# Kernel optimization log

Hardware: AMD Instinct MI355X
Metric: run time of the kernel (lower is better)

The kernel has to match this reference:

```python
import jax, jax.numpy as jnp
import numpy as np

N_CLASS, N_SUPPORT, N_QUERY = 64, 5, 64
D_IN, C, WIN = 1024, 128, 5
D = C * WIN * WIN  # 3200, fine-encoder output dim


def setup_inputs() -> dict:
    key = jax.random.key(0)
    ks = jax.random.split(key, 6)
    s = 0.02  # weight init scale
    return {
        "xs": jax.random.normal(ks[0], (N_CLASS, N_SUPPORT, D_IN), jnp.float32),
        "xq": jax.random.normal(ks[1], (N_CLASS, N_QUERY, D_IN), jnp.float32),
        "W_share": jax.random.normal(ks[2], (D_IN, D), jnp.float32) * s,
        "b_share": jnp.zeros((D,), jnp.float32),
        "W_att": jax.random.normal(ks[3], (C, C), jnp.float32) * s,
        "b_att": jnp.zeros((C,), jnp.float32),
        "W_fine": jax.random.normal(ks[4], (D, D), jnp.float32) * s,
        "b_fine": jnp.zeros((D,), jnp.float32),
    }


def reference(xs, xq, W_share, b_share, W_att, b_att, W_fine, b_fine):
    n_class, n_support = xs.shape[0], xs.shape[1]
    n_query = xq.shape[1]
    ns = n_class * n_support

    # concat support + query, run shared encoder
    x = jnp.concatenate([xs.reshape(ns, -1), xq.reshape(n_class * n_query, -1)], axis=0)
    z_share = jax.nn.relu(x @ W_share + b_share)            # [N, D]
    z4 = z_share.reshape(-1, C, WIN, WIN)

    # attention head: spatial mean -> linear -> per-channel logits
    z_att = z4.mean(axis=(2, 3)) @ W_att + b_att            # [N, C]

    diag_c = jax.nn.softmax(z_att[:ns].mean(axis=0)) * C    # [C]
    w = jnp.repeat(diag_c, WIN * WIN)                       # [D] diagonal of learned metric

    # fine encoder (flatten + linear)
    z = z_share @ W_fine + b_fine                           # [N, D]
    z_proto = z[:ns].reshape(n_class, n_support, -1).mean(axis=1)  # [n_class, D]
    zq = z[ns:]                                             # [n, D]

    # attentionMetric with diagonal metric == weighted squared distance:
    # dists[i,j] = sum_d w_d (zq_i - proto_j)^2, expanded to avoid the n*m*d diff tensor
    q2 = (zq * zq) @ w                                      # [n]
    p2 = (z_proto * z_proto) @ w                            # [m]
    cross = (zq * w) @ z_proto.T                            # [n, m]
    dists = q2[:, None] + p2[None, :] - 2.0 * cross         # [n, m]

    log_p_y = jax.nn.log_softmax(-dists, axis=1).reshape(n_class, n_query, n_class)
    target = jnp.arange(n_class)
    tgt = jnp.broadcast_to(target[:, None, None], (n_class, n_query, 1))
    loss_val = -jnp.take_along_axis(log_p_y, tgt, axis=2).mean()
    y_hat = jnp.argmax(log_p_y, axis=2)
    acc_val = (y_hat == target[:, None]).astype(jnp.float32).mean()
    return loss_val, acc_val
```

## Files before the change

kernel.cpp:

```cpp
#include <hip/hip_runtime.h>
#include <math.h>

#define N_CLASS 64
#define N_SUPPORT 5
#define N_QUERY 64
#define D_IN 1024
#define C_CH 128
#define WIN 5
#define D_FEAT 3200
#define NS 320
#define NQ 4096
#define M_ROWS 4416
#define M_PAD8 4608
#define N_PAD8 3328

#define ZP_SLICE  (N_CLASS * D_FEAT)
#define GT_SLICE  (128 * D_FEAT)
#define CR_SLICE  (NQ * 128)
#define NKS       10
#define LOSS_BLKS (NQ / 4)

#define PREP_X   4608
#define PREP_WS  3200
#define PREP_WZ  128
#define CONV_WF  10000

#define WS_SCALE    64.0f
#define WS_INVSCALE 0.015625f

#define WS_XF8      0u
#define WS_WSF8     4718592u
#define WS_ZSB      8126464u
#define WS_WFB      36388864u
#define WS_WFTB     56868864u
#define WS_ARENA    77348864u
#define WS_UB       98320384u
#define WS_YB       99139584u
#define WS_GT       99958784u
#define WS_WV       100777984u
#define WS_P2       100790784u
#define WS_CVEC     100791296u
#define WS_LPART    100791808u

typedef __bf16 bf16x8 __attribute__((ext_vector_type(8)));
typedef __bf16 bf16x4 __attribute__((ext_vector_type(4)));
typedef float floatx4 __attribute__((ext_vector_type(4)));
typedef __attribute__((address_space(1))) const void* gptr_t;
typedef __attribute__((address_space(3))) void* lptr_t;

__device__ __forceinline__ float waveReduceSum(float v) {
    for (int off = 32; off > 0; off >>= 1) v += __shfl_xor(v, off, 64);
    return v;
}

__global__ __launch_bounds__(256) void prep_kernel(const float* __restrict__ xs,
                                                   const float* __restrict__ xq,
                                                   const float* __restrict__ W_share,
                                                   unsigned char* __restrict__ Xf8,
                                                   unsigned char* __restrict__ Wsf8)
{
    __shared__ float tile[32][33];
    const int b = blockIdx.x;
    const int t = threadIdx.x;

    if (b < PREP_X) {
        const int e = (b * 256 + t) * 4;
        const int row = e >> 10;
        const int col = e & 1023;
        float4 v = make_float4(0.f, 0.f, 0.f, 0.f);
        if (row < NS)          v = *(const float4*)(xs + (size_t)row * D_IN + col);
        else if (row < M_ROWS) v = *(const float4*)(xq + (size_t)(row - NS) * D_IN + col);
        int p = __builtin_amdgcn_cvt_pk_fp8_f32(v.x, v.y, 0, false);
        p     = __builtin_amdgcn_cvt_pk_fp8_f32(v.z, v.w, p, true);
        const int ocol = col ^ (((row >> 1) & 1) << 3);
        *(int*)(Xf8 + (size_t)row * D_IN + ocol) = p;
        return;
    }
    if (b < PREP_X + PREP_WS) {
        const int tx = t & 31;
        const int ty = t >> 5;
        const int tb = b - PREP_X;
        const int n0 = (tb % 100) * 32;
        const int k0 = (tb / 100) * 32;
#pragma unroll
        for (int i = ty; i < 32; i += 8)
            tile[i][tx] = W_share[(size_t)(k0 + i) * D_FEAT + n0 + tx];
        __syncthreads();
#pragma unroll
        for (int i = ty; i < 32; i += 8) {
            const int p = __builtin_amdgcn_cvt_pk_fp8_f32(tile[tx][i] * WS_SCALE, 0.f,
                                                          0, false);
            const int n = n0 + i;
            const int k = (k0 + tx) ^ (((n >> 1) & 1) << 3);
            Wsf8[(size_t)n * D_IN + k] = (unsigned char)(p & 0xff);
        }
        return;
    }
    const int r = b - (PREP_X + PREP_WS);
    ((int*)(Wsf8 + (size_t)(3200 + r) * D_IN))[t] = 0;
}

__global__ __launch_bounds__(512, 2) void gemm_fp8_8p(const unsigned char* __restrict__ A,
                                                      const unsigned char* __restrict__ Bt,
                                                      const float* __restrict__ bias,
                                                      __bf16* __restrict__ out_bf)
{
    __shared__ __align__(16) unsigned char smem[131072];

    const int t    = threadIdx.x;
    const int lane = t & 63;
    const int w    = t >> 6;
    const int wm   = w >> 2;
    const int wn   = w & 3;

    const int bx = blockIdx.x % 13;
    const int by = blockIdx.x / 13;
    const int bm = by * 256;
    const int bn = bx * 256;

    const int q    = lane >> 4;
    const int r16  = lane & 15;
    const int m3   = (r16 >> 1) & 7;
    const int off0 = (q ^ m3) * 8;

    const int rowA = (wm * 128 + r16) * 64;
    const int rowB = (wn * 64 + r16) * 64;

    const int srow  = t >> 2;
    const int sunit = 16 * ((t & 3) ^ ((srow >> 2) & 3));

    auto stage_a = [&](int uu) {
        const unsigned char* g = A + (size_t)(bm + srow) * D_IN + uu * 64 + sunit;
        unsigned char* l = smem + (uu & 3) * 32768 + t * 16;
        __builtin_amdgcn_global_load_lds((gptr_t)g,            (lptr_t)l,          16, 0, 0);
        __builtin_amdgcn_global_load_lds((gptr_t)(g + 131072), (lptr_t)(l + 8192), 16, 0, 0);
    };
    auto stage_b = [&](int uu) {
        const unsigned char* g = Bt + (size_t)(bn + srow) * D_IN + uu * 64 + sunit;
        unsigned char* l = smem + (uu & 3) * 32768 + 16384 + t * 16;
        __builtin_amdgcn_global_load_lds((gptr_t)g,            (lptr_t)l,          16, 0, 0);
        __builtin_amdgcn_global_load_lds((gptr_t)(g + 131072), (lptr_t)(l + 8192), 16, 0, 0);
    };

    floatx4 acc[8][4] = {};
    long av[8], bv[4];

    auto ld_frags = [&](const unsigned char* sa, int o) {
        const unsigned char* sb = sa + 16384;
#pragma unroll
        for (int mi = 0; mi < 8; ++mi) av[mi] = *(const long*)(sa + rowA + mi * 1024 + o);
#pragma unroll
        for (int ni = 0; ni < 4; ++ni) bv[ni] = *(const long*)(sb + rowB + ni * 1024 + o);
    };
    auto do_mfma = [&]() {
        __builtin_amdgcn_s_barrier();
        asm volatile("s_waitcnt lgkmcnt(0)" ::: "memory");
        __builtin_amdgcn_s_setprio(1);
#pragma unroll
        for (int mi = 0; mi < 8; ++mi)
#pragma unroll
            for (int ni = 0; ni < 4; ++ni)
                acc[mi][ni] = __builtin_amdgcn_mfma_f32_16x16x32_fp8_fp8(
                    av[mi], bv[ni], acc[mi][ni], 0, 0, 0);
        __builtin_amdgcn_s_setprio(0);
        __builtin_amdgcn_s_barrier();
    };

    stage_a(0); stage_b(0);
    stage_a(1); stage_b(1);
    stage_a(2); stage_b(2);

    for (int u = 0; u < 13; ++u) {
        const unsigned char* sa = smem + (u & 3) * 32768;
        asm volatile("s_waitcnt vmcnt(8)" ::: "memory");
        __builtin_amdgcn_s_barrier();
        ld_frags(sa, off0);
        stage_a(u + 3);
        do_mfma();
        ld_frags(sa, off0 ^ 32);
        stage_b(u + 3);
        do_mfma();
    }
    asm volatile("s_waitcnt vmcnt(0)" ::: "memory");
    __builtin_amdgcn_s_barrier();
    for (int u = 13; u < 16; ++u) {
        const unsigned char* sa = smem + (u & 3) * 32768;
        ld_frags(sa, off0);
        do_mfma();
        ld_frags(sa, off0 ^ 32);
        do_mfma();
    }

#pragma unroll
    for (int ni = 0; ni < 4; ++ni) {
        const int col = bn + wn * 64 + ni * 16 + r16;
        if (col < D_FEAT) {
            const float bcol = bias[col];
#pragma unroll
            for (int mi = 0; mi < 8; ++mi) {
#pragma unroll
                for (int reg = 0; reg < 4; ++reg) {
                    const int row = bm + wm * 128 + mi * 16 + q * 4 + reg;
                    if (row < M_ROWS) {
                        float v = acc[mi][ni][reg] * WS_INVSCALE + bcol;
                        v = fmaxf(v, 0.f);
                        out_bf[(size_t)row * D_FEAT + col] = (__bf16)v;
                    }
                }
            }
        }
    }
}

__global__ __launch_bounds__(256) void gemm_bf16(const __bf16* __restrict__ A,
                                                 const __bf16* __restrict__ Bt,
                                                 const float* __restrict__ bias,
                                                 __bf16* __restrict__ out_bf,
                                                 float* __restrict__ out_f32,
                                                 int N, int strideK, int kIters,
                                                 int Mout, int relu, int sliceStride,
                                                 int nbx, int nby)
{
    __shared__ __align__(16) char smem[32768];

    int bx, by, ks;
    {
        const int nbxy = nbx * nby;
        ks = blockIdx.x / nbxy;
        const int b = blockIdx.x - ks * nbxy;
        const int fg = nbx >> 3;
        const int full = fg * 8 * nby;
        if (b < full) {
            const int g = b / (8 * nby);
            const int r = b - g * 8 * nby;
            bx = g * 8 + (r & 7);
            by = r >> 3;
        } else {
            const int rem = nbx - fg * 8;
            const int r = b - full;
            bx = fg * 8 + r % rem;
            by = r / rem;
        }
    }

    const int t    = threadIdx.x;
    const int lane = t & 63;
    const int w    = t >> 6;
    const int wm   = w >> 1;
    const int wn   = w & 1;
    const int bm   = by * 128;
    const int bn   = bx * 128;

    const int q    = lane >> 4;
    const int r16  = lane & 15;
    const int sw   = (r16 >> 1) & 3;
    const int cA   = (q ^ sw) * 8;

    const int srow   = w * 16 + (lane >> 2);
    const int sglob8 = (((lane & 3) ^ ((lane >> 3) & 3))) * 8;

    const int kBase = ks * kIters * 64;
    floatx4 acc[4][4] = {};

    for (int ki = 0; ki < kIters; ++ki) {
        const int k0 = kBase + ki * 64;
        __syncthreads();
#pragma unroll
        for (int s = 0; s < 2; ++s) {
#pragma unroll
            for (int j = 0; j < 2; ++j) {
                const __bf16* ga = A  + (size_t)(bm + j * 64 + srow) * strideK
                                      + k0 + s * 32 + sglob8;
                const __bf16* gb = Bt + (size_t)(bn + j * 64 + srow) * strideK
                                      + k0 + s * 32 + sglob8;
                char* la = smem +         s * 8192 + (j * 256 + w * 64) * 16;
                char* lb = smem + 16384 + s * 8192 + (j * 256 + w * 64) * 16;
                __builtin_amdgcn_global_load_lds((gptr_t)ga, (lptr_t)la, 16, 0, 0);
                __builtin_amdgcn_global_load_lds((gptr_t)gb, (lptr_t)lb, 16, 0, 0);
            }
        }
        __syncthreads();

#pragma unroll
        for (int s = 0; s < 2; ++s) {
            const __bf16* sAe = (const __bf16*)(smem +         s * 8192);
            const __bf16* sBe = (const __bf16*)(smem + 16384 + s * 8192);
            bf16x8 av[4], bv[4];
#pragma unroll
            for (int mi = 0; mi < 4; ++mi)
                av[mi] = *(const bf16x8*)(sAe + ((wm * 64 + mi * 16 + r16) * 32 + cA));
#pragma unroll
            for (int ni = 0; ni < 4; ++ni)
                bv[ni] = *(const bf16x8*)(sBe + ((wn * 64 + ni * 16 + r16) * 32 + cA));
#pragma unroll
            for (int mi = 0; mi < 4; ++mi)
#pragma unroll
                for (int ni = 0; ni < 4; ++ni)
                    acc[mi][ni] = __builtin_amdgcn_mfma_f32_16x16x32_bf16(
                        av[mi], bv[ni], acc[mi][ni], 0, 0, 0);
        }
    }

#pragma unroll
    for (int ni = 0; ni < 4; ++ni) {
        const int col = bn + wn * 64 + ni * 16 + r16;
        const float bcol = sliceStride ? 0.f : bias[col];
#pragma unroll
        for (int mi = 0; mi < 4; ++mi) {
#pragma unroll
            for (int reg = 0; reg < 4; ++reg) {
                const int row = bm + wm * 64 + mi * 16 + q * 4 + reg;
                if (row < Mout) {
                    if (sliceStride) {
                        out_f32[(size_t)ks * sliceStride + (size_t)row * N + col] =
                            acc[mi][ni][reg];
                    } else {
                        float v = acc[mi][ni][reg] + bcol;
                        if (relu) v = fmaxf(v, 0.f);
                        if (out_f32) out_f32[(size_t)row * N + col] = v;
                        else         out_bf [(size_t)row * N + col] = (__bf16)v;
                    }
                }
            }
        }
    }
}

__global__ __launch_bounds__(256) void ut_conv_kernel(const __bf16* __restrict__ z_share,
                                                      const float* __restrict__ W_fine,
                                                      __bf16* __restrict__ u,
                                                      float* __restrict__ upool,
                                                      __bf16* __restrict__ Wfb,
                                                      __bf16* __restrict__ WfTb)
{
    __shared__ __align__(16) char smem_u[D_FEAT * 4];
    const int b = blockIdx.x;
    const int t = threadIdx.x;

    if (b >= 128) {
        float (*tile)[33] = (float(*)[33])smem_u;
        const int tb = b - 128;
        const int tx = t & 31;
        const int ty = t >> 5;
        const int n0 = (tb % 100) * 32;
        const int k0 = (tb / 100) * 32;
#pragma unroll
        for (int i = ty; i < 32; i += 8) {
            const float v = W_fine[(size_t)(k0 + i) * D_FEAT + n0 + tx];
            Wfb[(size_t)(k0 + i) * D_FEAT + n0 + tx] = (__bf16)v;
            tile[i][tx] = v;
        }
        __syncthreads();
#pragma unroll
        for (int i = ty; i < 32; i += 8)
            WfTb[(size_t)(n0 + i) * D_FEAT + k0 + tx] = (__bf16)tile[tx][i];
        return;
    }

    float* srow_ = (float*)smem_u;
    const int p = b;
    if (p >= N_CLASS) {
        for (int k = t; k < D_FEAT; k += 256) u[(size_t)p * D_FEAT + k] = (__bf16)0.f;
        return;
    }
    const __bf16* base = z_share + (size_t)(p * N_SUPPORT) * D_FEAT;
    for (int k = t; k < D_FEAT; k += 256) {
        float s = 0.f;
#pragma unroll
        for (int ss = 0; ss < N_SUPPORT; ++ss) s += (float)base[(size_t)ss * D_FEAT + k];
        s *= (1.0f / N_SUPPORT);
        u[(size_t)p * D_FEAT + k] = (__bf16)s;
        srow_[k] = s;
    }
    __syncthreads();
    if (t < C_CH) {
        float pool = 0.f;
#pragma unroll
        for (int win = 0; win < 25; ++win) pool += srow_[t * 25 + win];
        upool[(size_t)p * C_CH + t] = pool;
    }
}

__global__ __launch_bounds__(128) void att2_kernel(const float* __restrict__ upool,
                                                   const float* __restrict__ W_att,
                                                   const float* __restrict__ b_att,
                                                   float* __restrict__ wvec)
{
    __shared__ float s_pm[C_CH];
    __shared__ float s_att[C_CH];
    __shared__ float s_diag[C_CH];
    const int c = threadIdx.x;
    float a = 0.f;
    for (int p = 0; p < N_CLASS; ++p) a += upool[(size_t)p * C_CH + c];
    s_pm[c] = a * (1.0f / (N_CLASS * 25));
    __syncthreads();
    float acc = b_att[c];
    for (int k = 0; k < C_CH; ++k) acc += s_pm[k] * W_att[k * C_CH + c];
    s_att[c] = acc;
    __syncthreads();
    float m = -INFINITY;
    for (int k = 0; k < C_CH; ++k) m = fmaxf(m, s_att[k]);
    float s = 0.f;
    for (int k = 0; k < C_CH; ++k) s += expf(s_att[k] - m);
    s_diag[c] = expf(acc - m) / s * (float)C_CH;
    __syncthreads();
    for (int j = c; j < D_FEAT; j += C_CH) wvec[j] = s_diag[j / 25];
}

__global__ __launch_bounds__(256) void y_kernel(const float* __restrict__ zp_part,
                                                const float* __restrict__ wv,
                                                const float* __restrict__ bf,
                                                __bf16* __restrict__ y,
                                                float* __restrict__ p2,
                                                float* __restrict__ cvec)
{
    __shared__ float s_red2[8];
    const int p = blockIdx.x;
    const int t = threadIdx.x;
    if (p >= N_CLASS) {
        for (int j = t; j < D_FEAT; j += 256) y[(size_t)p * D_FEAT + j] = (__bf16)0.f;
        return;
    }
    float s2 = 0.f, sc = 0.f;
    for (int j = t; j < D_FEAT; j += 256) {
        float zpf = bf[j];
#pragma unroll
        for (int ss = 0; ss < NKS; ++ss)
            zpf += zp_part[(size_t)ss * ZP_SLICE + (size_t)p * D_FEAT + j];
        const float wj = wv[j];
        y[(size_t)p * D_FEAT + j] = (__bf16)(wj * zpf);
        s2 += wj * zpf * zpf;
        sc += bf[j] * wj * zpf;
    }
    s2 = waveReduceSum(s2);
    sc = waveReduceSum(sc);
    const int lane = t & 63, wid = t >> 6;
    if (lane == 0) { s_red2[wid] = s2; s_red2[4 + wid] = sc; }
    __syncthreads();
    if (t == 0) {
        p2[p]   = s_red2[0] + s_red2[1] + s_red2[2] + s_red2[3];
        cvec[p] = s_red2[4] + s_red2[5] + s_red2[6] + s_red2[7];
    }
}

__global__ __launch_bounds__(256) void gtsum_kernel(const float* __restrict__ gp,
                                                    __bf16* __restrict__ Gt)
{
    const int i4 = blockIdx.x * 256 + threadIdx.x;
    if (i4 >= GT_SLICE / 4) return;
    float4 s = make_float4(0.f, 0.f, 0.f, 0.f);
#pragma unroll
    for (int ss = 0; ss < NKS; ++ss) {
        const float4 v = *(const float4*)(gp + (size_t)ss * GT_SLICE + i4 * 4);
        s.x += v.x; s.y += v.y; s.z += v.z; s.w += v.w;
    }
    bf16x4 o = { (__bf16)s.x, (__bf16)s.y, (__bf16)s.z, (__bf16)s.w };
    *(bf16x4*)(Gt + (size_t)i4 * 4) = o;
}

__global__ __launch_bounds__(256) void loss_kernel(const float* __restrict__ cross_part,
                                                   const float* __restrict__ p2,
                                                   const float* __restrict__ cvec,
                                                   float* __restrict__ lpart)
{
    __shared__ float s_l[4], s_a[4];
    const int t = threadIdx.x;
    const int lane = t & 63, wid = t >> 6;
    const int i = blockIdx.x * 4 + wid;
    float cr = 0.f;
#pragma unroll
    for (int ss = 0; ss < NKS; ++ss)
        cr += cross_part[(size_t)ss * CR_SLICE + (size_t)i * 128 + lane];
    const float neg = 2.0f * (cr + cvec[lane]) - p2[lane];
    float m = neg;
    for (int off = 32; off > 0; off >>= 1) m = fmaxf(m, __shfl_xor(m, off, 64));
    float e = expf(neg - m);
    float ssum = e;
    for (int off = 32; off > 0; off >>= 1) ssum += __shfl_xor(ssum, off, 64);
    const float lse = m + logf(ssum);
    const int tcls = i >> 6;
    const float negt = __shfl(neg, tcls, 64);
    float v = -neg; int bi = lane;
    for (int off = 32; off > 0; off >>= 1) {
        const float ov = __shfl_xor(v, off, 64);
        const int   oi = __shfl_xor(bi, off, 64);
        if (ov < v || (ov == v && oi < bi)) { v = ov; bi = oi; }
    }
    if (lane == 0) { s_l[wid] = lse - negt; s_a[wid] = (bi == tcls) ? 1.0f : 0.0f; }
    __syncthreads();
    if (t == 0) {
        lpart[blockIdx.x]             = s_l[0] + s_l[1] + s_l[2] + s_l[3];
        lpart[LOSS_BLKS + blockIdx.x] = s_a[0] + s_a[1] + s_a[2] + s_a[3];
    }
}

__global__ __launch_bounds__(256) void writeout_kernel(const float* __restrict__ lpart,
                                                       float* __restrict__ out)
{
    __shared__ float s_red2[8];
    const int t = threadIdx.x;
    float l = 0.f, a = 0.f;
    for (int k = t; k < LOSS_BLKS; k += 256) {
        l += lpart[k];
        a += lpart[LOSS_BLKS + k];
    }
    l = waveReduceSum(l);
    a = waveReduceSum(a);
    const int lane = t & 63, wid = t >> 6;
    if (lane == 0) { s_red2[wid] = l; s_red2[4 + wid] = a; }
    __syncthreads();
    if (t == 0) {
        out[0] = (s_red2[0] + s_red2[1] + s_red2[2] + s_red2[3]) * (1.0f / NQ);
        out[1] = (s_red2[4] + s_red2[5] + s_red2[6] + s_red2[7]) * (1.0f / NQ);
    }
}

extern "C" void kernel_launch(void* const* d_in, const int* in_sizes, int n_in,
                              void* d_out, int out_size, void* d_ws, size_t ws_size,
                              hipStream_t stream)
{
    const float* xs      = (const float*)d_in[0];
    const float* xq      = (const float*)d_in[1];
    const float* W_share = (const float*)d_in[2];
    const float* b_share = (const float*)d_in[3];
    const float* W_att   = (const float*)d_in[4];
    const float* b_att   = (const float*)d_in[5];
    const float* W_fine  = (const float*)d_in[6];
    const float* b_fine  = (const float*)d_in[7];
    float* out = (float*)d_out;

    char* ws = (char*)d_ws;
    unsigned char* Xf8  = (unsigned char*)(ws + WS_XF8);
    unsigned char* Wsf8 = (unsigned char*)(ws + WS_WSF8);
    __bf16* Zsb     = (__bf16*)(ws + WS_ZSB);
    __bf16* Wfb     = (__bf16*)(ws + WS_WFB);
    __bf16* WfTb    = (__bf16*)(ws + WS_WFTB);
    float*  arena   = (float*) (ws + WS_ARENA);
    float*  upool   = arena;
    float*  zp_part = arena;
    float*  gt_part = arena;
    float*  cr_part = arena;
    __bf16* ub      = (__bf16*)(ws + WS_UB);
    __bf16* yb      = (__bf16*)(ws + WS_YB);
    __bf16* Gt      = (__bf16*)(ws + WS_GT);
    float*  wv      = (float*) (ws + WS_WV);
    float*  p2v     = (float*) (ws + WS_P2);
    float*  cvec    = (float*) (ws + WS_CVEC);
    float*  lpart   = (float*) (ws + WS_LPART);

    prep_kernel<<<PREP_X + PREP_WS + PREP_WZ, 256, 0, stream>>>(xs, xq, W_share,
                                                                Xf8, Wsf8);

    gemm_fp8_8p<<<18 * 13, 512, 0, stream>>>(Xf8, Wsf8, b_share, Zsb);

    ut_conv_kernel<<<128 + CONV_WF, 256, 0, stream>>>(Zsb, W_fine, ub, upool,
                                                      Wfb, WfTb);
    att2_kernel<<<1, C_CH, 0, stream>>>(upool, W_att, b_att, wv);

    gemm_bf16<<<25 * NKS, 256, 0, stream>>>(
        ub, WfTb, nullptr, nullptr, zp_part,
        D_FEAT, D_FEAT, 5, N_CLASS, 0, ZP_SLICE, 25, 1);

    y_kernel<<<128, 256, 0, stream>>>(zp_part, wv, b_fine, yb, p2v, cvec);

    gemm_bf16<<<25 * NKS, 256, 0, stream>>>(
        yb, Wfb, nullptr, nullptr, gt_part,
        D_FEAT, D_FEAT, 5, 128, 0, GT_SLICE, 25, 1);

    gtsum_kernel<<<(GT_SLICE / 4 + 255) / 256, 256, 0, stream>>>(gt_part, Gt);

    gemm_bf16<<<32 * NKS, 256, 0, stream>>>(
        Zsb + (size_t)NS * D_FEAT, Gt, nullptr, nullptr, cr_part,
        128, D_FEAT, 5, NQ, 0, CR_SLICE, 1, 32);

    loss_kernel<<<LOSS_BLKS, 256, 0, stream>>>(cr_part, p2v, cvec, lpart);

    writeout_kernel<<<1, 256, 0, stream>>>(lpart, out);
}
```

Baseline: 253.7 us.

## Retile FP8 shared-encoder GEMM to 128x128 blocks with LDS-staged coalesced epilogue

```diff
diff --git a/kernel.cpp b/kernel.cpp
--- a/kernel.cpp
+++ b/kernel.cpp
@@ -11,8 +11,7 @@
 #define NS 320
 #define NQ 4096
 #define M_ROWS 4416
-#define M_PAD8 4608
-#define N_PAD8 3328
+#define M_PAD 4480
 
 #define ZP_SLICE  (N_CLASS * D_FEAT)
 #define GT_SLICE  (128 * D_FEAT)
@@ -20,9 +19,8 @@
 #define NKS       10
 #define LOSS_BLKS (NQ / 4)
 
-#define PREP_X   4608
+#define PREP_X   4480
 #define PREP_WS  3200
-#define PREP_WZ  128
 #define CONV_WF  10000
 
 #define WS_SCALE    64.0f
@@ -76,138 +74,154 @@
         *(int*)(Xf8 + (size_t)row * D_IN + ocol) = p;
         return;
     }
-    if (b < PREP_X + PREP_WS) {
-        const int tx = t & 31;
-        const int ty = t >> 5;
-        const int tb = b - PREP_X;
-        const int n0 = (tb % 100) * 32;
-        const int k0 = (tb / 100) * 32;
-#pragma unroll
-        for (int i = ty; i < 32; i += 8)
-            tile[i][tx] = W_share[(size_t)(k0 + i) * D_FEAT + n0 + tx];
-        __syncthreads();
-#pragma unroll
-        for (int i = ty; i < 32; i += 8) {
-            const int p = __builtin_amdgcn_cvt_pk_fp8_f32(tile[tx][i] * WS_SCALE, 0.f,
-                                                          0, false);
-            const int n = n0 + i;
-            const int k = (k0 + tx) ^ (((n >> 1) & 1) << 3);
-            Wsf8[(size_t)n * D_IN + k] = (unsigned char)(p & 0xff);
-        }
-        return;
-    }
-    const int r = b - (PREP_X + PREP_WS);
-    ((int*)(Wsf8 + (size_t)(3200 + r) * D_IN))[t] = 0;
-}
-
-__global__ __launch_bounds__(512, 2) void gemm_fp8_8p(const unsigned char* __restrict__ A,
-                                                      const unsigned char* __restrict__ Bt,
-                                                      const float* __restrict__ bias,
-                                                      __bf16* __restrict__ out_bf)
-{
-    __shared__ __align__(16) unsigned char smem[131072];
+    const int tx = t & 31;
+    const int ty = t >> 5;
+    const int tb = b - PREP_X;
+    const int n0 = (tb % 100) * 32;
+    const int k0 = (tb / 100) * 32;
+#pragma unroll
+    for (int i = ty; i < 32; i += 8)
+        tile[i][tx] = W_share[(size_t)(k0 + i) * D_FEAT + n0 + tx];
+    __syncthreads();
+#pragma unroll
+    for (int i = ty; i < 32; i += 8) {
+        const int p = __builtin_amdgcn_cvt_pk_fp8_f32(tile[tx][i] * WS_SCALE, 0.f,
+                                                      0, false);
+        const int n = n0 + i;
+        const int k = (k0 + tx) ^ (((n >> 1) & 1) << 3);
+        Wsf8[(size_t)n * D_IN + k] = (unsigned char)(p & 0xff);
+    }
+}
+
+__global__ __launch_bounds__(256, 3) void gemm_fp8_128(const unsigned char* __restrict__ A,
+                                                       const unsigned char* __restrict__ Bt,
+                                                       const float* __restrict__ bias,
+                                                       __bf16* __restrict__ out_bf)
+{
+    __shared__ __align__(16) unsigned char smem[49152];
 
     const int t    = threadIdx.x;
     const int lane = t & 63;
     const int w    = t >> 6;
-    const int wm   = w >> 2;
-    const int wn   = w & 3;
-
-    const int bx = blockIdx.x % 13;
-    const int by = blockIdx.x / 13;
-    const int bm = by * 256;
-    const int bn = bx * 256;
+    const int wm   = w >> 1;
+    const int wn   = w & 1;
+
+    const int bx = blockIdx.x % 25;
+    const int by = blockIdx.x / 25;
+    const int bm = by * 128;
+    const int bn = bx * 128;
 
     const int q    = lane >> 4;
     const int r16  = lane & 15;
     const int m3   = (r16 >> 1) & 7;
     const int off0 = (q ^ m3) * 8;
 
-    const int rowA = (wm * 128 + r16) * 64;
+    const int rowA = (wm * 64 + r16) * 64;
     const int rowB = (wn * 64 + r16) * 64;
 
     const int srow  = t >> 2;
     const int sunit = 16 * ((t & 3) ^ ((srow >> 2) & 3));
 
-    auto stage_a = [&](int uu) {
-        const unsigned char* g = A + (size_t)(bm + srow) * D_IN + uu * 64 + sunit;
-        unsigned char* l = smem + (uu & 3) * 32768 + t * 16;
-        __builtin_amdgcn_global_load_lds((gptr_t)g,            (lptr_t)l,          16, 0, 0);
-        __builtin_amdgcn_global_load_lds((gptr_t)(g + 131072), (lptr_t)(l + 8192), 16, 0, 0);
+    const unsigned char* gA = A  + (size_t)(bm + srow) * D_IN + sunit;
+    const unsigned char* gB = Bt + (size_t)(bn + srow) * D_IN + sunit;
+
+    auto stage = [&](int uu, int slot) {
+        const unsigned char* ga = gA + uu * 64;
+        const unsigned char* gb = gB + uu * 64;
+        unsigned char* l = smem + slot * 16384 + t * 16;
+        __builtin_amdgcn_global_load_lds((gptr_t)ga,           (lptr_t)l,            16, 0, 0);
+        __builtin_amdgcn_global_load_lds((gptr_t)(ga + 65536), (lptr_t)(l + 4096),   16, 0, 0);
+        __builtin_amdgcn_global_load_lds((gptr_t)gb,           (lptr_t)(l + 8192),   16, 0, 0);
+        __builtin_amdgcn_global_load_lds((gptr_t)(gb + 65536), (lptr_t)(l + 12288),  16, 0, 0);
     };
-    auto stage_b = [&](int uu) {
-        const unsigned char* g = Bt + (size_t)(bn + srow) * D_IN + uu * 64 + sunit;
-        unsigned char* l = smem + (uu & 3) * 32768 + 16384 + t * 16;
-        __builtin_amdgcn_global_load_lds((gptr_t)g,            (lptr_t)l,          16, 0, 0);
-        __builtin_amdgcn_global_load_lds((gptr_t)(g + 131072), (lptr_t)(l + 8192), 16, 0, 0);
+
+    floatx4 acc[4][4] = {};
+    long av[4], bv[4];
+
+    auto ld_frags = [&](const unsigned char* sa, int o) {
+#pragma unroll
+        for (int mi = 0; mi < 4; ++mi)
+            av[mi] = *(const long*)(sa + rowA + mi * 1024 + o);
+#pragma unroll
+        for (int ni = 0; ni < 4; ++ni)
+            bv[ni] = *(const long*)(sa + 8192 + rowB + ni * 1024 + o);
     };
-
-    floatx4 acc[8][4] = {};
-    long av[8], bv[4];
-
-    auto ld_frags = [&](const unsigned char* sa, int o) {
-        const unsigned char* sb = sa + 16384;
-#pragma unroll
-        for (int mi = 0; mi < 8; ++mi) av[mi] = *(const long*)(sa + rowA + mi * 1024 + o);
-#pragma unroll
-        for (int ni = 0; ni < 4; ++ni) bv[ni] = *(const long*)(sb + rowB + ni * 1024 + o);
+    auto mfma16 = [&]() {
+#pragma unroll
+        for (int mi = 0; mi < 4; ++mi)
+#pragma unroll
+            for (int ni = 0; ni < 4; ++ni)
+                acc[mi][ni] = __builtin_amdgcn_mfma_f32_16x16x32_fp8_fp8(
+                    av[mi], bv[ni], acc[mi][ni], 0, 0, 0);
     };
-    auto do_mfma = [&]() {
+
+    stage(0, 0);
+    stage(1, 1);
+    asm volatile("s_waitcnt vmcnt(4)" ::: "memory");
+    __builtin_amdgcn_s_barrier();
+
+    int sl = 0;
+    for (int u = 0; u < 14; ++u) {
+        const unsigned char* sa = smem + sl * 16384;
+        ld_frags(sa, off0);
+        stage(u + 2, sl == 0 ? 2 : sl - 1);
         __builtin_amdgcn_s_barrier();
         asm volatile("s_waitcnt lgkmcnt(0)" ::: "memory");
         __builtin_amdgcn_s_setprio(1);
-#pragma unroll
-        for (int mi = 0; mi < 8; ++mi)
-#pragma unroll
-            for (int ni = 0; ni < 4; ++ni)
-                acc[mi][ni] = __builtin_amdgcn_mfma_f32_16x16x32_fp8_fp8(
-                    av[mi], bv[ni], acc[mi][ni], 0, 0, 0);
+        mfma16();
         __builtin_amdgcn_s_setprio(0);
         __builtin_amdgcn_s_barrier();
-    };
-
-    stage_a(0); stage_b(0);
-    stage_a(1); stage_b(1);
-    stage_a(2); stage_b(2);
-
-    for (int u = 0; u < 13; ++u) {
-        const unsigned char* sa = smem + (u & 3) * 32768;
-        asm volatile("s_waitcnt vmcnt(8)" ::: "memory");
+        ld_frags(sa, off0 ^ 32);
+        asm volatile("s_waitcnt vmcnt(4)" ::: "memory");
         __builtin_amdgcn_s_barrier();
-        ld_frags(sa, off0);
-        stage_a(u + 3);
-        do_mfma();
-        ld_frags(sa, off0 ^ 32);
-        stage_b(u + 3);
-        do_mfma();
+        asm volatile("s_waitcnt lgkmcnt(0)" ::: "memory");
+        __builtin_amdgcn_s_setprio(1);
+        mfma16();
+        __builtin_amdgcn_s_setprio(0);
+        __builtin_amdgcn_s_barrier();
+        sl = sl == 2 ? 0 : sl + 1;
+    }
+    {
+        const unsigned char* sa = smem + sl * 16384;
+        ld_frags(sa, off0);       mfma16();
+        ld_frags(sa, off0 ^ 32);  mfma16();
+        sl = sl == 2 ? 0 : sl + 1;
     }
     asm volatile("s_waitcnt vmcnt(0)" ::: "memory");
     __builtin_amdgcn_s_barrier();
-    for (int u = 13; u < 16; ++u) {
-        const unsigned char* sa = smem + (u & 3) * 32768;
-        ld_frags(sa, off0);
-        do_mfma();
-        ld_frags(sa, off0 ^ 32);
-        do_mfma();
-    }
-
-#pragma unroll
-    for (int ni = 0; ni < 4; ++ni) {
-        const int col = bn + wn * 64 + ni * 16 + r16;
-        if (col < D_FEAT) {
-            const float bcol = bias[col];
-#pragma unroll
-            for (int mi = 0; mi < 8; ++mi) {
-#pragma unroll
-                for (int reg = 0; reg < 4; ++reg) {
-                    const int row = bm + wm * 128 + mi * 16 + q * 4 + reg;
-                    if (row < M_ROWS) {
-                        float v = acc[mi][ni][reg] * WS_INVSCALE + bcol;
-                        v = fmaxf(v, 0.f);
-                        out_bf[(size_t)row * D_FEAT + col] = (__bf16)v;
-                    }
-                }
+    {
+        const unsigned char* sa = smem + sl * 16384;
+        ld_frags(sa, off0);       mfma16();
+        ld_frags(sa, off0 ^ 32);  mfma16();
+    }
+
+    __syncthreads();
+    float bcol[4];
+#pragma unroll
+    for (int ni = 0; ni < 4; ++ni) bcol[ni] = bias[bn + wn * 64 + ni * 16 + r16];
+    const int ebase = (wm * 64 + q * 4) * 256 + wn * 128 + r16 * 2;
+#pragma unroll
+    for (int mi = 0; mi < 4; ++mi)
+#pragma unroll
+        for (int ni = 0; ni < 4; ++ni) {
+            const int cb = (ni ^ q) << 5;
+#pragma unroll
+            for (int reg = 0; reg < 4; ++reg) {
+                float v = acc[mi][ni][reg] * WS_INVSCALE + bcol[ni];
+                v = fmaxf(v, 0.f);
+                *(__bf16*)(smem + ebase + mi * 4096 + reg * 256 + cb) = (__bf16)v;
             }
+        }
+    __syncthreads();
+#pragma unroll
+    for (int ps = 0; ps < 8; ++ps) {
+        const int idx  = ps * 256 + t;
+        const int row  = idx >> 4;
+        const int grow = bm + row;
+        if (grow < M_ROWS) {
+            const int lb = row * 256 + (((idx & 15) << 4) ^ (((row >> 2) & 3) << 5));
+            const int4 d = *(const int4*)(smem + lb);
+            *(int4*)((char*)out_bf + ((size_t)grow * D_FEAT + bn + (idx & 15) * 8) * 2) = d;
         }
     }
 }
@@ -548,10 +562,9 @@
     float*  cvec    = (float*) (ws + WS_CVEC);
     float*  lpart   = (float*) (ws + WS_LPART);
 
-    prep_kernel<<<PREP_X + PREP_WS + PREP_WZ, 256, 0, stream>>>(xs, xq, W_share,
-                                                                Xf8, Wsf8);
-
-    gemm_fp8_8p<<<18 * 13, 512, 0, stream>>>(Xf8, Wsf8, b_share, Zsb);
+    prep_kernel<<<PREP_X + PREP_WS, 256, 0, stream>>>(xs, xq, W_share, Xf8, Wsf8);
+
+    gemm_fp8_128<<<35 * 25, 256, 0, stream>>>(Xf8, Wsf8, b_share, Zsb);
 
     ut_conv_kernel<<<128 + CONV_WF, 256, 0, stream>>>(Zsb, W_fine, ub, upool,
                                                       Wfb, WfTb);
```

New measurement: 238.0 us. -6.2%, faster.
